# Performance work log

Measured on AMD Instinct MI355X. Metric: run time of the kernel, lower is better.

The kernel has to match this reference:

```python
import jax, jax.numpy as jnp
import numpy as np

GROUPS = 2
STRIDE = (1, 1)
PADDING = ((1, 1), (1, 1))
DILATION = (1, 1)


def setup_inputs() -> dict:
    key = jax.random.key(0)
    k1, k2, k3 = jax.random.split(key, 3)
    B, Cin, H, W = 16, 256, 112, 112
    Cout, kH, kW = 256, 3, 3
    x = jax.random.normal(k1, (B, Cin, H, W), dtype=jnp.float32)
    # kaiming_uniform-like scale: fan_in = (Cin/groups)*kH*kW
    fan_in = (Cin // GROUPS) * kH * kW
    bound = float(np.sqrt(1.0 / fan_in))
    weight = jax.random.uniform(k2, (Cout, Cin // GROUPS, kH, kW), dtype=jnp.float32,
                                minval=-bound, maxval=bound)
    bias = jax.random.uniform(k3, (Cout,), dtype=jnp.float32, minval=-bound, maxval=bound)
    return {"x": x, "weight": weight, "bias": bias}


def reference(x, weight, bias):
    # Grouped conv2d: every backend path of SparseGroupedConv2d (sparse triton
    # active-tile kernel, zero-tile skip, dense F.conv2d fallback) computes this
    # exact grouped convolution; the tile machinery only skips zero-energy tiles.
    y = jax.lax.conv_general_dilated(
        x, weight,
        window_strides=STRIDE,
        padding=PADDING,
        rhs_dilation=DILATION,
        dimension_numbers=("NCHW", "OIHW", "NCHW"),
        feature_group_count=GROUPS,
    )
    return y + bias[None, :, None, None]
```

## Files before the change

kernel.cpp:

```cpp
#include <hip/hip_runtime.h>
#include <hip/hip_bf16.h>
#include <stdint.h>

#define BATCH 16
#define CIN   256
#define HH    112
#define WW    112
#define GROUPS 2
#define CG    128
#define COG   128
#define RH    4
#define CK    32
#define NCHUNK (CG/CK)

typedef __bf16 bf16x8 __attribute__((ext_vector_type(8)));
typedef float  f32x4  __attribute__((ext_vector_type(4)));

#define WB_BYTES   (GROUPS*3*3*COG*CG*2)
#define ZBUF_OFF   WB_BYTES
#define ZBUF_BYTES 8192
#define XB_OFF     (ZBUF_OFF + ZBUF_BYTES)
#define XB_BYTES   ((size_t)BATCH*HH*WW*CIN*2)
#define WS_NEED    ((size_t)XB_OFF + XB_BYTES)

__device__ inline void load_lds16(const void* g, void* l) {
    __builtin_amdgcn_global_load_lds(
        (const __attribute__((address_space(1))) void*)g,
        (__attribute__((address_space(3))) void*)l, 16, 0, 0);
}

__global__ __launch_bounds__(256) void k_wcvt(const float* __restrict__ w,
                                              ushort* __restrict__ wb) {
    int i = blockIdx.x * 256 + threadIdx.x;
    int ci = i & 127;
    int t  = i >> 7;
    int co = t & 127;
    t >>= 7;
    int kw = t % 3; t /= 3;
    int kh = t % 3;
    int g  = t / 3;
    int src = (((g*COG + co)*CG + ci)*3 + kh)*3 + kw;
    __hip_bfloat16 v = __float2bfloat16(w[src]);
    wb[i] = *reinterpret_cast<ushort*>(&v);
}

#define XPAD 113
__global__ __launch_bounds__(256) void k_xcvt(const float* __restrict__ x,
                                              ushort* __restrict__ xb) {
    __shared__ float tile[64 * XPAD];
    int bid = blockIdx.x;
    int cc  = bid & 3;
    int h   = (bid >> 2) % HH;
    int b   = bid / (4 * HH);
    int tid = threadIdx.x;

    const float* src = x + ((size_t)(b*CIN + cc*64) * HH + h) * WW;
    for (int tt = tid; tt < 64*28; tt += 256) {
        int c = tt / 28, v = tt % 28;
        float4 f = *reinterpret_cast<const float4*>(src + (size_t)c*HH*WW + v*4);
        float* d = &tile[c*XPAD + v*4];
        d[0]=f.x; d[1]=f.y; d[2]=f.z; d[3]=f.w;
    }
    __syncthreads();

    if (tid < 224) {
        int w = tid >> 1, half = tid & 1;
        ushort o[32];
#pragma unroll
        for (int j = 0; j < 32; ++j) {
            __hip_bfloat16 v = __float2bfloat16(tile[(half*32 + j)*XPAD + w]);
            o[j] = *reinterpret_cast<ushort*>(&v);
        }
        ushort* dst = xb + (((size_t)(b*HH + h)*WW + w)*CIN + cc*64 + half*32);
        const uint4* o4 = reinterpret_cast<const uint4*>(o);
        uint4* d4 = reinterpret_cast<uint4*>(dst);
        d4[0]=o4[0]; d4[1]=o4[1]; d4[2]=o4[2]; d4[3]=o4[3];
    }
}

__device__ inline void stage_w_all(const ushort* __restrict__ wb, ushort* wsb,
                                   int g, int chunk, int wave, int lane) {
    int co = wave*16 + (lane >> 2);
    int t  = (lane & 3) ^ ((lane >> 3) & 3);
#pragma unroll
    for (int tap = 0; tap < 9; ++tap) {
        const ushort* src = wb + (((size_t)(g*9 + tap)*COG + co)*CG + chunk*CK + t*8);
        load_lds16(src, wsb + (tap*COG + wave*16)*CK);
    }
}

__device__ inline void stage_x(const ushort* __restrict__ xb, ushort* dst,
                               const ushort* __restrict__ zbuf,
                               int b, int g, int oh0, int chunk, int wave, int lane) {
    int qv = lane >> 2;
    for (int t = wave; t < 42; t += 8) {
        int rr = t / 7, ii = t % 7;
        int h    = oh0 - 1 + rr;
        int w_in = ii*16 + qv;
        int ts   = (lane & 3) ^ (((2*rr + 1 + qv) >> 1) & 3);
        const ushort* src = (h >= 0 && h < HH)
            ? xb + (((size_t)(b*HH + h)*WW + w_in)*CIN + g*CG + chunk*CK + ts*8)
            : zbuf + lane*8;
        load_lds16(src, dst + (rr*114 + 1 + ii*16)*CK);
    }
}

__global__ __launch_bounds__(512, 2) void k_conv(const ushort* __restrict__ xb,
                                                 const ushort* __restrict__ wb,
                                                 const float* __restrict__ bias,
                                                 float* __restrict__ out,
                                                 const ushort* __restrict__ zbuf) {
    __shared__ __align__(16) ushort xs[2][6*114*CK];
    __shared__ __align__(16) ushort wsb[9*COG*CK];

    int bid = blockIdx.x;
    int g   = bid / 448;
    int r   = bid % 448;
    int b   = r / 28;
    int q   = r % 28;
    int oh0 = q * RH;

    int tid  = threadIdx.x;
    int wave = tid >> 6;
    int lane = tid & 63;
    int wm   = wave >> 2;
    int wr   = wave & 3;
    int l15  = lane & 15;
    int lk   = lane >> 4;

    for (int t = tid; t < 768; t += 512) {
        int buf = t / 384, r2 = t % 384;
        int rr = r2 / 64, wcol = (r2 >> 5) & 1, c = r2 & 31;
        xs[buf][(rr*114 + wcol*113)*CK + c] = 0;
    }

    int sA = lk ^ ((l15 >> 1) & 3);

    f32x4 acc[4][7];
#pragma unroll
    for (int m = 0; m < 4; ++m)
#pragma unroll
        for (int n = 0; n < 7; ++n) acc[m][n] = f32x4{0.f,0.f,0.f,0.f};

    stage_x(xb, xs[0], zbuf, b, g, oh0, 0, wave, lane);
    stage_w_all(wb, wsb, g, 0, wave, lane);
    __syncthreads();

#pragma unroll 1
    for (int c = 0; c < NCHUNK; ++c) {
        const ushort* xcur = xs[c & 1];
        if (c + 1 < NCHUNK)
            stage_x(xb, xs[(c + 1) & 1], zbuf, b, g, oh0, c + 1, wave, lane);

#pragma unroll
        for (int kkw = 0; kkw < 9; ++kkw) {
            const int kh = kkw / 3, kw = kkw - kh*3;
            int sB = lk ^ (((2*(wr + kh) + l15 + kw) >> 1) & 3);
            const ushort* bbase = &xcur[((wr + kh)*114 + l15 + kw)*CK + sB*8];
            bf16x8 bfr[7];
#pragma unroll
            for (int n = 0; n < 7; ++n)
                bfr[n] = *reinterpret_cast<const bf16x8*>(bbase + n*16*CK);

            const ushort* abase = &wsb[(kkw*COG + wm*64 + l15)*CK + sA*8];
#pragma unroll
            for (int m = 0; m < 4; ++m) {
                bf16x8 afr = *reinterpret_cast<const bf16x8*>(abase + m*16*CK);
#pragma unroll
                for (int n = 0; n < 7; ++n)
                    acc[m][n] = __builtin_amdgcn_mfma_f32_16x16x32_bf16(
                        afr, bfr[n], acc[m][n], 0, 0, 0);
            }
        }

        __builtin_amdgcn_sched_barrier(0);
        asm volatile("s_waitcnt lgkmcnt(0)" ::: "memory");
        __builtin_amdgcn_s_barrier();

        if (c + 1 < NCHUNK)
            stage_w_all(wb, wsb, g, c + 1, wave, lane);

        __syncthreads();
    }

    int oh = oh0 + wr;
#pragma unroll
    for (int m = 0; m < 4; ++m) {
        int cob = g*CG + wm*64 + m*16 + lk*4;
#pragma unroll
        for (int j = 0; j < 4; ++j) {
            int co = cob + j;
            float bv = bias[co];
            float* orow = out + (((size_t)(b*CIN + co)*HH + oh)*WW);
#pragma unroll
            for (int n = 0; n < 7; ++n)
                orow[n*16 + l15] = acc[m][n][j] + bv;
        }
    }
}

__global__ __launch_bounds__(128) void k_direct(const float* __restrict__ x,
                                                const float* __restrict__ w,
                                                const float* __restrict__ bias,
                                                float* __restrict__ out) {
    int bid = blockIdx.x;
    int oh  = bid % HH;
    int t   = bid / HH;
    int co  = t % CIN;
    int b   = t / CIN;
    int ow  = threadIdx.x;
    if (ow >= WW) return;
    int g = co / COG;
    float s = bias[co];
    const float* wp = w + (size_t)co*CG*9;
    const float* xp = x + ((size_t)b*CIN + g*CG)*HH*WW;
    for (int ci = 0; ci < CG; ++ci) {
        const float* xr = xp + (size_t)ci*HH*WW;
        const float* wr_ = wp + ci*9;
#pragma unroll
        for (int kh = 0; kh < 3; ++kh) {
            int ih = oh + kh - 1;
            if (ih < 0 || ih >= HH) continue;
#pragma unroll
            for (int kw = 0; kw < 3; ++kw) {
                int iw = ow + kw - 1;
                if (iw < 0 || iw >= WW) continue;
                s += xr[ih*WW + iw] * wr_[kh*3 + kw];
            }
        }
    }
    out[(((size_t)b*CIN + co)*HH + oh)*WW + ow] = s;
}

extern "C" void kernel_launch(void* const* d_in, const int* in_sizes, int n_in,
                              void* d_out, int out_size, void* d_ws, size_t ws_size,
                              hipStream_t stream) {
    const float* x    = (const float*)d_in[0];
    const float* w    = (const float*)d_in[1];
    const float* bias = (const float*)d_in[2];
    float* out        = (float*)d_out;

    if (ws_size >= WS_NEED) {
        ushort* wb   = (ushort*)d_ws;
        ushort* zb   = (ushort*)((char*)d_ws + ZBUF_OFF);
        ushort* xbuf = (ushort*)((char*)d_ws + XB_OFF);
        hipMemsetAsync(zb, 0, ZBUF_BYTES, stream);
        k_wcvt<<<1152, 256, 0, stream>>>(w, wb);
        k_xcvt<<<BATCH*HH*4, 256, 0, stream>>>(x, xbuf);
        k_conv<<<896, 512, 0, stream>>>(xbuf, wb, bias, out, zb);
    } else {
        k_direct<<<BATCH*CIN*HH, 128, 0, stream>>>(x, w, bias, out);
    }
}
```

Measured before the change: 225.1 us.

## Persistent-style conv blocks with fine-grained double-buffered weight and input staging

```diff
diff --git a/kernel.cpp b/kernel.cpp
--- a/kernel.cpp
+++ b/kernel.cpp
@@ -9,7 +9,6 @@
 #define GROUPS 2
 #define CG    128
 #define COG   128
-#define RH    4
 #define CK    32
 #define NCHUNK (CG/CK)
 
@@ -78,123 +77,152 @@
     }
 }
 
-__device__ inline void stage_w_all(const ushort* __restrict__ wb, ushort* wsb,
-                                   int g, int chunk, int wave, int lane) {
+__device__ inline void stage_w3(const ushort* __restrict__ wb, ushort* dstbuf,
+                                int g, int tap_base, int cin, int wave, int lane) {
     int co = wave*16 + (lane >> 2);
-    int t  = (lane & 3) ^ ((lane >> 3) & 3);
-#pragma unroll
-    for (int tap = 0; tap < 9; ++tap) {
-        const ushort* src = wb + (((size_t)(g*9 + tap)*COG + co)*CG + chunk*CK + t*8);
-        load_lds16(src, wsb + (tap*COG + wave*16)*CK);
-    }
-}
-
-__device__ inline void stage_x(const ushort* __restrict__ xb, ushort* dst,
-                               const ushort* __restrict__ zbuf,
-                               int b, int g, int oh0, int chunk, int wave, int lane) {
+    int ts = (lane & 3) ^ ((lane >> 3) & 3);
+#pragma unroll
+    for (int i = 0; i < 3; ++i) {
+        const ushort* src = wb + (((size_t)(g*9 + tap_base + i)*COG + co)*CG + cin + ts*8);
+        load_lds16(src, dstbuf + (i*COG + wave*16)*CK);
+    }
+}
+
+__device__ inline void xpre_task(const ushort* __restrict__ xb, ushort* dstbuf,
+                                 const ushort* __restrict__ zbuf,
+                                 int b, int g, int oh0n, int cin, int t, int lane) {
+    int rr = t / 7, ii = t % 7;
+    int h  = oh0n - 1 + rr;
     int qv = lane >> 2;
-    for (int t = wave; t < 42; t += 8) {
-        int rr = t / 7, ii = t % 7;
-        int h    = oh0 - 1 + rr;
-        int w_in = ii*16 + qv;
-        int ts   = (lane & 3) ^ (((2*rr + 1 + qv) >> 1) & 3);
-        const ushort* src = (h >= 0 && h < HH)
-            ? xb + (((size_t)(b*HH + h)*WW + w_in)*CIN + g*CG + chunk*CK + ts*8)
-            : zbuf + lane*8;
-        load_lds16(src, dst + (rr*114 + 1 + ii*16)*CK);
-    }
-}
+    int w_in = ii*16 + qv;
+    int ts = (lane & 3) ^ (((2*rr + 1 + qv) >> 1) & 3);
+    const ushort* src = (h >= 0 && h < HH)
+        ? xb + (((size_t)(b*HH + h)*WW + w_in)*CIN + g*CG + cin + ts*8)
+        : zbuf + lane*8;
+    load_lds16(src, dstbuf + (rr*114 + 1 + ii*16)*CK);
+}
+
+#define PHASE(KH, KW, XCUR, WBUF)                                           \
+  {                                                                         \
+    int sB = lk ^ (((2*(wr + (KH)) + l15 + (KW)) >> 1) & 3);                \
+    const ushort* bbase = (XCUR) + ((wr + (KH))*114 + l15 + (KW))*CK + sB*8;\
+    bf16x8 bfr[7];                                                          \
+    _Pragma("unroll")                                                       \
+    for (int n = 0; n < 7; ++n)                                             \
+      bfr[n] = *reinterpret_cast<const bf16x8*>(bbase + n*16*CK);           \
+    const ushort* abase = (WBUF) + ((KW)*COG + wm*32 + l15)*CK + sA*8;      \
+    __builtin_amdgcn_s_setprio(1);                                          \
+    _Pragma("unroll")                                                       \
+    for (int m = 0; m < 2; ++m) {                                           \
+      bf16x8 afr = *reinterpret_cast<const bf16x8*>(abase + m*16*CK);       \
+      _Pragma("unroll")                                                     \
+      for (int n = 0; n < 7; ++n)                                           \
+        acc[m][n] = __builtin_amdgcn_mfma_f32_16x16x32_bf16(                \
+            afr, bfr[n], acc[m][n], 0, 0, 0);                               \
+    }                                                                       \
+    __builtin_amdgcn_s_setprio(0);                                          \
+  }
+
+#define GROUP3(KH, XCUR, WBUF)   \
+    PHASE(KH, 0, XCUR, WBUF)     \
+    PHASE(KH, 1, XCUR, WBUF)     \
+    PHASE(KH, 2, XCUR, WBUF)
 
 __global__ __launch_bounds__(512, 2) void k_conv(const ushort* __restrict__ xb,
                                                  const ushort* __restrict__ wb,
                                                  const float* __restrict__ bias,
                                                  float* __restrict__ out,
                                                  const ushort* __restrict__ zbuf) {
-    __shared__ __align__(16) ushort xs[2][6*114*CK];
-    __shared__ __align__(16) ushort wsb[9*COG*CK];
-
-    int bid = blockIdx.x;
-    int g   = bid / 448;
-    int r   = bid % 448;
-    int b   = r / 28;
-    int q   = r % 28;
-    int oh0 = q * RH;
+    __shared__ __align__(16) ushort xs[2][4*114*CK];
+    __shared__ __align__(16) ushort wsb[2][3*COG*CK];
+
+    int g    = blockIdx.x >> 7;
+    int rem  = blockIdx.x & 127;
+    int b    = rem >> 3;
+    int q0   = (rem & 7) * 7;
 
     int tid  = threadIdx.x;
     int wave = tid >> 6;
     int lane = tid & 63;
-    int wm   = wave >> 2;
-    int wr   = wave & 3;
+    int wm   = wave >> 1;
+    int wr   = wave & 1;
     int l15  = lane & 15;
     int lk   = lane >> 4;
-
-    for (int t = tid; t < 768; t += 512) {
-        int buf = t / 384, r2 = t % 384;
-        int rr = r2 / 64, wcol = (r2 >> 5) & 1, c = r2 & 31;
-        xs[buf][(rr*114 + wcol*113)*CK + c] = 0;
-    }
-
-    int sA = lk ^ ((l15 >> 1) & 3);
-
-    f32x4 acc[4][7];
-#pragma unroll
-    for (int m = 0; m < 4; ++m)
+    int sA   = lk ^ ((l15 >> 1) & 3);
+
+    {
+        int buf = tid >> 8, r2 = (tid >> 6) & 3, wc = (tid >> 5) & 1, ch = tid & 31;
+        xs[buf][(r2*114 + wc*113)*CK + ch] = 0;
+    }
+
+    float breg[2][4];
+#pragma unroll
+    for (int m = 0; m < 2; ++m)
+#pragma unroll
+        for (int j = 0; j < 4; ++j)
+            breg[m][j] = bias[g*COG + wm*32 + m*16 + lk*4 + j];
+
+    f32x4 acc[2][7];
+#pragma unroll
+    for (int m = 0; m < 2; ++m)
 #pragma unroll
         for (int n = 0; n < 7; ++n) acc[m][n] = f32x4{0.f,0.f,0.f,0.f};
 
-    stage_x(xb, xs[0], zbuf, b, g, oh0, 0, wave, lane);
-    stage_w_all(wb, wsb, g, 0, wave, lane);
+    for (int t = wave; t < 28; t += 8)
+        xpre_task(xb, xs[0], zbuf, b, g, 2*q0, 0, t, lane);
+    stage_w3(wb, wsb[0], g, 0, 0, wave, lane);
     __syncthreads();
 
 #pragma unroll 1
-    for (int c = 0; c < NCHUNK; ++c) {
-        const ushort* xcur = xs[c & 1];
-        if (c + 1 < NCHUNK)
-            stage_x(xb, xs[(c + 1) & 1], zbuf, b, g, oh0, c + 1, wave, lane);
-
-#pragma unroll
-        for (int kkw = 0; kkw < 9; ++kkw) {
-            const int kh = kkw / 3, kw = kkw - kh*3;
-            int sB = lk ^ (((2*(wr + kh) + l15 + kw) >> 1) & 3);
-            const ushort* bbase = &xcur[((wr + kh)*114 + l15 + kw)*CK + sB*8];
-            bf16x8 bfr[7];
-#pragma unroll
-            for (int n = 0; n < 7; ++n)
-                bfr[n] = *reinterpret_cast<const bf16x8*>(bbase + n*16*CK);
-
-            const ushort* abase = &wsb[(kkw*COG + wm*64 + l15)*CK + sA*8];
-#pragma unroll
-            for (int m = 0; m < 4; ++m) {
-                bf16x8 afr = *reinterpret_cast<const bf16x8*>(abase + m*16*CK);
-#pragma unroll
-                for (int n = 0; n < 7; ++n)
-                    acc[m][n] = __builtin_amdgcn_mfma_f32_16x16x32_bf16(
-                        afr, bfr[n], acc[m][n], 0, 0, 0);
+    for (int CC = 0; CC < 28; ++CC) {
+        int e    = CC >> 2;
+        int oh0  = 2*(q0 + e);
+        int p0   = CC & 1;
+        const ushort* xcur = xs[p0];
+        int cin  = (CC & 3) * CK;
+        int cinN = ((CC + 1) & 3) * CK;
+        int oh0n = 2*(q0 + ((CC + 1) >> 2));
+
+        stage_w3(wb, wsb[p0^1], g, 3, cin, wave, lane);
+        if (CC < 27) {
+            xpre_task(xb, xs[p0^1], zbuf, b, g, oh0n, cinN, wave,     lane);
+            xpre_task(xb, xs[p0^1], zbuf, b, g, oh0n, cinN, wave + 8, lane);
+        }
+        GROUP3(0, xcur, wsb[p0])
+        __syncthreads();
+
+        stage_w3(wb, wsb[p0], g, 6, cin, wave, lane);
+        if (CC < 27) {
+            xpre_task(xb, xs[p0^1], zbuf, b, g, oh0n, cinN, wave + 16, lane);
+            if (wave + 24 < 28)
+                xpre_task(xb, xs[p0^1], zbuf, b, g, oh0n, cinN, wave + 24, lane);
+        }
+        GROUP3(1, xcur, wsb[p0^1])
+        __syncthreads();
+
+        if (CC < 27)
+            stage_w3(wb, wsb[p0^1], g, 0, cinN, wave, lane);
+        GROUP3(2, xcur, wsb[p0])
+        __syncthreads();
+
+        if ((CC & 3) == 3) {
+            int oh = oh0 + wr;
+#pragma unroll
+            for (int m = 0; m < 2; ++m) {
+                int co = g*COG + wm*32 + m*16 + lk*4;
+#pragma unroll
+                for (int j = 0; j < 4; ++j) {
+                    float bv = breg[m][j];
+                    float* orow = out + (((size_t)(b*CIN + co + j)*HH + oh)*WW);
+#pragma unroll
+                    for (int n = 0; n < 7; ++n)
+                        orow[n*16 + l15] = acc[m][n][j] + bv;
+                }
             }
-        }
-
-        __builtin_amdgcn_sched_barrier(0);
-        asm volatile("s_waitcnt lgkmcnt(0)" ::: "memory");
-        __builtin_amdgcn_s_barrier();
-
-        if (c + 1 < NCHUNK)
-            stage_w_all(wb, wsb, g, c + 1, wave, lane);
-
-        __syncthreads();
-    }
-
-    int oh = oh0 + wr;
-#pragma unroll
-    for (int m = 0; m < 4; ++m) {
-        int cob = g*CG + wm*64 + m*16 + lk*4;
-#pragma unroll
-        for (int j = 0; j < 4; ++j) {
-            int co = cob + j;
-            float bv = bias[co];
-            float* orow = out + (((size_t)(b*CIN + co)*HH + oh)*WW);
-#pragma unroll
-            for (int n = 0; n < 7; ++n)
-                orow[n*16 + l15] = acc[m][n][j] + bv;
+#pragma unroll
+            for (int m = 0; m < 2; ++m)
+#pragma unroll
+                for (int n = 0; n < 7; ++n) acc[m][n] = f32x4{0.f,0.f,0.f,0.f};
         }
     }
 }
@@ -247,7 +275,7 @@
         hipMemsetAsync(zb, 0, ZBUF_BYTES, stream);
         k_wcvt<<<1152, 256, 0, stream>>>(w, wb);
         k_xcvt<<<BATCH*HH*4, 256, 0, stream>>>(x, xbuf);
-        k_conv<<<896, 512, 0, stream>>>(xbuf, wb, bias, out, zb);
+        k_conv<<<256, 512, 0, stream>>>(xbuf, wb, bias, out, zb);
     } else {
         k_direct<<<BATCH*CIN*HH, 128, 0, stream>>>(x, w, bias, out);
     }
```

New measurement: 226.4 us. About the same (+0.6%).

## Software-pipeline conv LDS fragment loads, swap MFMA operands, vectorize stores, remap blocks

Applied to the files above, without the earlier changes.

```diff
diff --git a/kernel.cpp b/kernel.cpp
--- a/kernel.cpp
+++ b/kernel.cpp
@@ -9,9 +9,8 @@
 #define GROUPS 2
 #define CG    128
 #define COG   128
-#define RH    4
 #define CK    32
-#define NCHUNK (CG/CK)
+#define NCHUNK 4
 
 typedef __bf16 bf16x8 __attribute__((ext_vector_type(8)));
 typedef float  f32x4  __attribute__((ext_vector_type(4)));
@@ -78,20 +77,20 @@
     }
 }
 
-__device__ inline void stage_w_all(const ushort* __restrict__ wb, ushort* wsb,
-                                   int g, int chunk, int wave, int lane) {
+__device__ inline void stage_w_all(const ushort* __restrict__ wb, ushort* dstbuf,
+                                   int g, int cin, int wave, int lane) {
     int co = wave*16 + (lane >> 2);
-    int t  = (lane & 3) ^ ((lane >> 3) & 3);
+    int ts = (lane & 3) ^ ((lane >> 3) & 3);
 #pragma unroll
     for (int tap = 0; tap < 9; ++tap) {
-        const ushort* src = wb + (((size_t)(g*9 + tap)*COG + co)*CG + chunk*CK + t*8);
-        load_lds16(src, wsb + (tap*COG + wave*16)*CK);
+        const ushort* src = wb + (((size_t)(g*9 + tap)*COG + co)*CG + cin + ts*8);
+        load_lds16(src, dstbuf + (tap*COG + wave*16)*CK);
     }
 }
 
 __device__ inline void stage_x(const ushort* __restrict__ xb, ushort* dst,
                                const ushort* __restrict__ zbuf,
-                               int b, int g, int oh0, int chunk, int wave, int lane) {
+                               int b, int g, int oh0, int cin, int wave, int lane) {
     int qv = lane >> 2;
     for (int t = wave; t < 42; t += 8) {
         int rr = t / 7, ii = t % 7;
@@ -99,11 +98,38 @@
         int w_in = ii*16 + qv;
         int ts   = (lane & 3) ^ (((2*rr + 1 + qv) >> 1) & 3);
         const ushort* src = (h >= 0 && h < HH)
-            ? xb + (((size_t)(b*HH + h)*WW + w_in)*CIN + g*CG + chunk*CK + ts*8)
+            ? xb + (((size_t)(b*HH + h)*WW + w_in)*CIN + g*CG + cin + ts*8)
             : zbuf + lane*8;
         load_lds16(src, dst + (rr*114 + 1 + ii*16)*CK);
     }
 }
+
+#define XL(XN, KH2, KW2)                                                    \
+  {                                                                         \
+    int sB_ = lk ^ (((2*(wr + (KH2)) + l15 + (KW2)) >> 1) & 3);             \
+    const ushort* bb_ = xcur + ((wr + (KH2))*114 + l15 + (KW2))*CK + sB_*8; \
+    _Pragma("unroll")                                                       \
+    for (int n_ = 0; n_ < 7; ++n_)                                          \
+      XN[n_] = *reinterpret_cast<const bf16x8*>(bb_ + n_*16*CK);            \
+  }
+
+#define WL(TAP2)                                                            \
+  {                                                                         \
+    const ushort* ab_ = wsb + ((TAP2)*COG + wm*64 + l15)*CK + sA*8;         \
+    _Pragma("unroll")                                                       \
+    for (int u_ = 0; u_ < 4; ++u_)                                          \
+      wf[u_] = *reinterpret_cast<const bf16x8*>(ab_ + u_*16*CK);            \
+  }
+
+#define MF(XC)                                                              \
+    __builtin_amdgcn_s_setprio(1);                                          \
+    _Pragma("unroll")                                                       \
+    for (int u_ = 0; u_ < 4; ++u_)                                          \
+      _Pragma("unroll")                                                     \
+      for (int i_ = 0; i_ < 7; ++i_)                                        \
+        acc[i_][u_] = __builtin_amdgcn_mfma_f32_16x16x32_bf16(              \
+            XC[i_], wf[u_], acc[i_][u_], 0, 0, 0);                          \
+    __builtin_amdgcn_s_setprio(0);
 
 __global__ __launch_bounds__(512, 2) void k_conv(const ushort* __restrict__ xb,
                                                  const ushort* __restrict__ wb,
@@ -113,12 +139,12 @@
     __shared__ __align__(16) ushort xs[2][6*114*CK];
     __shared__ __align__(16) ushort wsb[9*COG*CK];
 
-    int bid = blockIdx.x;
-    int g   = bid / 448;
-    int r   = bid % 448;
+    int orig = (blockIdx.x & 7) * 112 + (blockIdx.x >> 3);
+    int g   = orig / 448;
+    int r   = orig % 448;
     int b   = r / 28;
     int q   = r % 28;
-    int oh0 = q * RH;
+    int oh0 = q * 4;
 
     int tid  = threadIdx.x;
     int wave = tid >> 6;
@@ -127,20 +153,26 @@
     int wr   = wave & 3;
     int l15  = lane & 15;
     int lk   = lane >> 4;
+    int sA   = lk ^ ((l15 >> 1) & 3);
 
     for (int t = tid; t < 768; t += 512) {
         int buf = t / 384, r2 = t % 384;
-        int rr = r2 / 64, wcol = (r2 >> 5) & 1, c = r2 & 31;
-        xs[buf][(rr*114 + wcol*113)*CK + c] = 0;
-    }
-
-    int sA = lk ^ ((l15 >> 1) & 3);
-
-    f32x4 acc[4][7];
-#pragma unroll
-    for (int m = 0; m < 4; ++m)
-#pragma unroll
-        for (int n = 0; n < 7; ++n) acc[m][n] = f32x4{0.f,0.f,0.f,0.f};
+        int rr = r2 / 64, wc = (r2 >> 5) & 1, ch = r2 & 31;
+        xs[buf][(rr*114 + wc*113)*CK + ch] = 0;
+    }
+
+    float bvreg[4];
+#pragma unroll
+    for (int u = 0; u < 4; ++u)
+        bvreg[u] = bias[g*COG + wm*64 + u*16 + l15];
+
+    f32x4 acc[7][4];
+#pragma unroll
+    for (int i = 0; i < 7; ++i)
+#pragma unroll
+        for (int u = 0; u < 4; ++u) acc[i][u] = f32x4{0.f,0.f,0.f,0.f};
+
+    bf16x8 xfA[7], xfB[7], wf[4];
 
     stage_x(xb, xs[0], zbuf, b, g, oh0, 0, wave, lane);
     stage_w_all(wb, wsb, g, 0, wave, lane);
@@ -150,51 +182,43 @@
     for (int c = 0; c < NCHUNK; ++c) {
         const ushort* xcur = xs[c & 1];
         if (c + 1 < NCHUNK)
-            stage_x(xb, xs[(c + 1) & 1], zbuf, b, g, oh0, c + 1, wave, lane);
-
-#pragma unroll
-        for (int kkw = 0; kkw < 9; ++kkw) {
-            const int kh = kkw / 3, kw = kkw - kh*3;
-            int sB = lk ^ (((2*(wr + kh) + l15 + kw) >> 1) & 3);
-            const ushort* bbase = &xcur[((wr + kh)*114 + l15 + kw)*CK + sB*8];
-            bf16x8 bfr[7];
-#pragma unroll
-            for (int n = 0; n < 7; ++n)
-                bfr[n] = *reinterpret_cast<const bf16x8*>(bbase + n*16*CK);
-
-            const ushort* abase = &wsb[(kkw*COG + wm*64 + l15)*CK + sA*8];
-#pragma unroll
-            for (int m = 0; m < 4; ++m) {
-                bf16x8 afr = *reinterpret_cast<const bf16x8*>(abase + m*16*CK);
-#pragma unroll
-                for (int n = 0; n < 7; ++n)
-                    acc[m][n] = __builtin_amdgcn_mfma_f32_16x16x32_bf16(
-                        afr, bfr[n], acc[m][n], 0, 0, 0);
-            }
-        }
+            stage_x(xb, xs[(c + 1) & 1], zbuf, b, g, oh0, (c + 1)*CK, wave, lane);
+
+        XL(xfA, 0, 0)
+        XL(xfB, 0, 1)  WL(0)  MF(xfA)
+        XL(xfA, 0, 2)  WL(1)  MF(xfB)
+        XL(xfB, 1, 0)  WL(2)  MF(xfA)
+        XL(xfA, 1, 1)  WL(3)  MF(xfB)
+        XL(xfB, 1, 2)  WL(4)  MF(xfA)
+        XL(xfA, 2, 0)  WL(5)  MF(xfB)
+        XL(xfB, 2, 1)  WL(6)  MF(xfA)
+        XL(xfA, 2, 2)  WL(7)  MF(xfB)
+                       WL(8)  MF(xfA)
 
         __builtin_amdgcn_sched_barrier(0);
         asm volatile("s_waitcnt lgkmcnt(0)" ::: "memory");
         __builtin_amdgcn_s_barrier();
 
         if (c + 1 < NCHUNK)
-            stage_w_all(wb, wsb, g, c + 1, wave, lane);
+            stage_w_all(wb, wsb, g, (c + 1)*CK, wave, lane);
 
         __syncthreads();
     }
 
     int oh = oh0 + wr;
 #pragma unroll
-    for (int m = 0; m < 4; ++m) {
-        int cob = g*CG + wm*64 + m*16 + lk*4;
-#pragma unroll
-        for (int j = 0; j < 4; ++j) {
-            int co = cob + j;
-            float bv = bias[co];
-            float* orow = out + (((size_t)(b*CIN + co)*HH + oh)*WW);
-#pragma unroll
-            for (int n = 0; n < 7; ++n)
-                orow[n*16 + l15] = acc[m][n][j] + bv;
+    for (int u = 0; u < 4; ++u) {
+        int co = g*COG + wm*64 + u*16 + l15;
+        float bv = bvreg[u];
+        float* obase = out + (((size_t)(b*CIN + co)*HH + oh)*WW + lk*4);
+#pragma unroll
+        for (int i = 0; i < 7; ++i) {
+            f32x4 v;
+            v[0] = acc[i][u][0] + bv;
+            v[1] = acc[i][u][1] + bv;
+            v[2] = acc[i][u][2] + bv;
+            v[3] = acc[i][u][3] + bv;
+            *reinterpret_cast<f32x4*>(obase + i*16) = v;
         }
     }
 }
```

Result: slower. 243.0 us (+8.0%).
